# Kernel optimization log

Hardware: AMD Instinct MI355X
Metric: run time of the kernel (lower is better)

## Reference

```python
import jax, jax.numpy as jnp
import numpy as np

B, T = 16, 512          # batch, timesteps
IN = 16                 # input_path_dim
D = 128                 # cde_state_dim
H = 256                 # vf_hidden_dim
L = 136                 # logsig_size = 16 + 16*15/2 (depth-2 log-signature)
O = 32                  # output_path_dim


def _linear_params(key, out_f, in_f):
    kw, kb = jax.random.split(key)
    lim = 1.0 / np.sqrt(in_f)
    W = jax.random.uniform(kw, (out_f, in_f), minval=-lim, maxval=lim, dtype=jnp.float32)
    b = jax.random.uniform(kb, (out_f,), minval=-lim, maxval=lim, dtype=jnp.float32)
    return W, b


def setup_inputs() -> dict:
    key = jax.random.key(0)
    ks = jax.random.split(key, 10)
    x0 = jax.random.normal(ks[0], (B, IN), dtype=jnp.float32)
    # log-signature increments are small; scale down for numerical realism
    logsigs = jax.random.normal(ks[1], (B, T - 1, L), dtype=jnp.float32) * 0.01
    # initial MLP: IN -> H -> H -> D (softplus activations, linear final)
    iw1, ib1 = _linear_params(ks[2], H, IN)
    iw2, ib2 = _linear_params(ks[3], H, H)
    iw3, ib3 = _linear_params(ks[4], D, H)
    # vector-field MLP: D -> H -> H -> D*L (softplus, tanh final)
    fw1, fb1 = _linear_params(ks[5], H, D)
    fw2, fb2 = _linear_params(ks[6], H, H)
    fw3, fb3 = _linear_params(ks[7], D * L, H)
    # readout: D -> O
    rw, rb = _linear_params(ks[8], O, D)
    return dict(x0=x0, logsigs=logsigs,
                iw1=iw1, ib1=ib1, iw2=iw2, ib2=ib2, iw3=iw3, ib3=ib3,
                fw1=fw1, fb1=fb1, fw2=fw2, fb2=fb2, fw3=fw3, fb3=fb3,
                rw=rw, rb=rb)


def reference(x0, logsigs, iw1, ib1, iw2, ib2, iw3, ib3,
              fw1, fb1, fw2, fb2, fw3, fb3, rw, rb):
    sp = jax.nn.softplus
    # initial MLP -> h0: (B, D)
    h0 = sp(x0 @ iw1.T + ib1)
    h0 = sp(h0 @ iw2.T + ib2)
    h0 = h0 @ iw3.T + ib3

    def step(h, logsig_t):
        # vector-field MLP: (B, D) -> (B, D*L), tanh final activation
        z = sp(h @ fw1.T + fb1)
        z = sp(z @ fw2.T + fb2)
        z = jnp.tanh(z @ fw3.T + fb3)
        mat = z.reshape(h.shape[0], D, L)          # (B, D, L)
        h_next = h + jnp.einsum('bdl,bl->bd', mat, logsig_t)
        return h_next, h_next

    # scan over time: xs shape (T-1, B, L)
    _, h_hist = jax.lax.scan(step, h0, jnp.swapaxes(logsigs, 0, 1))
    h_all = jnp.concatenate([h0[None, :, :], h_hist], axis=0)  # (T, B, D)
    out = h_all @ rw.T + rb                                     # (T, B, O)
    return jnp.swapaxes(out, 0, 1)                              # (B, T, O)
```

## Files before the change

kernel.cpp:

```cpp
#include <hip/hip_runtime.h>

namespace {
constexpr int kB = 16, kT = 512, kIN = 16, kD = 128, kH = 256, kL = 136, kO = 32;
constexpr int kSteps = kT - 1;
constexpr int NBLK = 256;
constexpr int NTHR = 512;
constexpr int LH   = 68;
constexpr int NTILE = 5;
constexpr int FS   = 32;
constexpr int OFF_FW1 = 0;
constexpr int OFF_FW2 = 32768;
constexpr int OFF_AHI = 98304;
constexpr int OFF_ALO = 106752;
constexpr int OFF_DT  = 115200;
constexpr int OFF_OMS = 120576;
constexpr int OFF_Z1S = 124928;
constexpr int OFF_HB  = 125952;
constexpr int OFF_RED = 126464;
constexpr size_t LDS_BYTES = 126976;
}

typedef __attribute__((ext_vector_type(8))) short short8;
typedef __attribute__((ext_vector_type(4))) float f32x4;

__device__ __forceinline__ float softplusf(float x) {
  return fmaxf(x, 0.0f) + log1pf(expf(-fabsf(x)));
}
__device__ __forceinline__ unsigned short f2bf(float x) {
  unsigned u = __float_as_uint(x);
  return (unsigned short)((u + 0x7FFFu + ((u >> 16) & 1u)) >> 16);
}
__device__ __forceinline__ float bf2f(unsigned short h) {
  return __uint_as_float(((unsigned)h) << 16);
}
#define ALOADF(p)  __hip_atomic_load((p),  __ATOMIC_RELAXED, __HIP_MEMORY_SCOPE_AGENT)
#define ASTOREF(p,v) __hip_atomic_store((p), (v), __ATOMIC_RELAXED, __HIP_MEMORY_SCOPE_AGENT)

__global__ void __launch_bounds__(256)
rde_init(const float* __restrict__ x0,
         const float* __restrict__ iw1, const float* __restrict__ ib1,
         const float* __restrict__ iw2, const float* __restrict__ ib2,
         const float* __restrict__ iw3, const float* __restrict__ ib3,
         float* __restrict__ hist) {
  __shared__ float xs[kIN];
  __shared__ __align__(16) float t1[kH];
  __shared__ __align__(16) float t2[kH];
  const int b = blockIdx.x, tid = threadIdx.x;
  if (tid < kIN) xs[tid] = x0[b*kIN + tid];
  __syncthreads();
  {
    float a = ib1[tid];
#pragma unroll
    for (int i = 0; i < kIN; ++i) a = fmaf(xs[i], iw1[tid*kIN + i], a);
    t1[tid] = softplusf(a);
  }
  __syncthreads();
  {
    const float4* wr = (const float4*)(iw2 + (size_t)tid*kH);
    float a = ib2[tid];
#pragma unroll 8
    for (int q = 0; q < kH/4; ++q) {
      float4 w = wr[q];
      a = fmaf(t1[4*q+0], w.x, a); a = fmaf(t1[4*q+1], w.y, a);
      a = fmaf(t1[4*q+2], w.z, a); a = fmaf(t1[4*q+3], w.w, a);
    }
    t2[tid] = softplusf(a);
  }
  __syncthreads();
  if (tid < kD) {
    const float4* wr = (const float4*)(iw3 + (size_t)tid*kH);
    float a = ib3[tid];
#pragma unroll 8
    for (int q = 0; q < kH/4; ++q) {
      float4 w = wr[q];
      a = fmaf(t2[4*q+0], w.x, a); a = fmaf(t2[4*q+1], w.y, a);
      a = fmaf(t2[4*q+2], w.z, a); a = fmaf(t2[4*q+3], w.w, a);
    }
    hist[(size_t)b*kD + tid] = a;
  }
}

__global__ void __launch_bounds__(NTHR, 2)
rde_scan(const float* __restrict__ lsg,
         const float* __restrict__ fw1, const float* __restrict__ fb1,
         const float* __restrict__ fw2, const float* __restrict__ fb2,
         const float* __restrict__ fw3, const float* __restrict__ fb3,
         float* __restrict__ hist, float* z1g, float* z2g, float* partg,
         unsigned* z1fl, unsigned* z2fl, unsigned* pfl) {
  extern __shared__ char smem[];
  float* fw1s = (float*)(smem + OFF_FW1);
  float* fw2s = (float*)(smem + OFF_FW2);
  unsigned short* Ahi = (unsigned short*)(smem + OFF_AHI);
  unsigned short* Alo = (unsigned short*)(smem + OFF_ALO);
  float* Dt  = (float*)(smem + OFF_DT);
  float* oms = (float*)(smem + OFF_OMS);
  float* z1s = (float*)(smem + OFF_Z1S);
  float* hb  = (float*)(smem + OFF_HB);
  float* red = (float*)(smem + OFF_RED);

  const int tid  = threadIdx.x;
  const int k    = blockIdx.x;
  const int wave = tid >> 6, lane = tid & 63;
  const int d_own = k >> 1, l0 = (k & 1) * LH;
  const bool isMLP = (k < 64);
  const int bmlp = k >> 2, qm = k & 3, j0 = qm * 64;

  short8 bhi[8], blo[8];
  float biasv = 0.f;
  {
#pragma unroll
    for (int s = 0; s < 8; ++s) { bhi[s] = (short8)0; blo[s] = (short8)0; }
    if (wave < NTILE) {
      const int nl = wave*16 + (lane & 15);
      const int g  = lane >> 4;
      if (nl < LH) {
        const size_t row = (size_t)d_own*kL + l0 + nl;
        const float* wrow = fw3 + row*kH;
        biasv = fb3[row];
#pragma unroll
        for (int s = 0; s < 8; ++s) {
          const int k0 = s*32 + g*8;
          float4 v0 = *(const float4*)(wrow + k0);
          float4 v1 = *(const float4*)(wrow + k0 + 4);
          float vv[8] = {v0.x,v0.y,v0.z,v0.w,v1.x,v1.y,v1.z,v1.w};
#pragma unroll
          for (int e = 0; e < 8; ++e) {
            unsigned short hh = f2bf(vv[e]);
            bhi[s][e] = (short)hh;
            blo[s][e] = (short)f2bf(vv[e] - bf2f(hh));
          }
        }
      }
    }
  }
  float myfb1 = 0.f, myfb2 = 0.f;
  if (isMLP) {
    if (tid < 256) { int j = tid >> 2; myfb1 = fb1[j0 + j]; myfb2 = fb2[j0 + j]; }
    for (int i = tid; i < 64*32; i += NTHR) {
      int j = i >> 5, qq = i & 31;
      float4 v = *(const float4*)(fw1 + (size_t)(j0 + j)*kD + qq*4);
      fw1s[(qq*4+0)*64 + j] = v.x; fw1s[(qq*4+1)*64 + j] = v.y;
      fw1s[(qq*4+2)*64 + j] = v.z; fw1s[(qq*4+3)*64 + j] = v.w;
    }
    for (int i = tid; i < 64*64; i += NTHR) {
      int j = i >> 6, qq = i & 63;
      float4 v = *(const float4*)(fw2 + (size_t)(j0 + j)*kH + qq*4);
      fw2s[(qq*4+0)*64 + j] = v.x; fw2s[(qq*4+1)*64 + j] = v.y;
      fw2s[(qq*4+2)*64 + j] = v.z; fw2s[(qq*4+3)*64 + j] = v.w;
    }
    for (int i = tid; i < kD; i += NTHR) hb[i] = hist[(size_t)bmlp*kD + i];
  }
  __syncthreads();

  for (int t = 0; t < kSteps; ++t) {
    const unsigned epw = (unsigned)(t + 1);

    if (tid >= 256) {
      int c = tid - 256;
#pragma unroll 2
      for (int rep = 0; rep < 2; ++rep) {
        int cc = c + rep*256;
        if (cc < 272) {
          int bb = cc / 17, ii = cc % 17;
          float4 v = *(const float4*)(lsg + ((size_t)bb*kSteps + t)*kL + l0 + ii*4);
          *(float4*)(oms + bb*LH + ii*4) = v;
        }
      }
    }

    if (isMLP) {
      if (tid < 256) {
        int j = tid >> 2, ks = tid & 3;
        float a = 0.f;
#pragma unroll 8
        for (int kk = ks; kk < kD; kk += 4) a = fmaf(hb[kk], fw1s[kk*64 + j], a);
        a += __shfl_xor(a, 1); a += __shfl_xor(a, 2);
        if (ks == 0) ASTOREF(z1g + bmlp*kH + j0 + j, softplusf(a + myfb1));
      }
      __syncthreads();
      if (tid == 0) __hip_atomic_store(z1fl + (bmlp*4 + qm)*FS, epw,
                                       __ATOMIC_RELAXED, __HIP_MEMORY_SCOPE_AGENT);
      if (tid < 4) {
        while (__hip_atomic_load(z1fl + (bmlp*4 + tid)*FS, __ATOMIC_RELAXED,
                                 __HIP_MEMORY_SCOPE_AGENT) < epw)
          __builtin_amdgcn_s_sleep(1);
      }
      __syncthreads();
      asm volatile("" ::: "memory");
      if (tid < 128) {
        unsigned long long v = __hip_atomic_load((const unsigned long long*)(z1g + bmlp*kH) + tid,
                                                 __ATOMIC_RELAXED, __HIP_MEMORY_SCOPE_AGENT);
        union { unsigned long long u; float2 f; } cv; cv.u = v;
        z1s[2*tid] = cv.f.x; z1s[2*tid + 1] = cv.f.y;
      }
      __syncthreads();
      if (tid < 256) {
        int j = tid >> 2, ks = tid & 3;
        float a = 0.f;
#pragma unroll 8
        for (int kk = ks; kk < kH; kk += 4) a = fmaf(z1s[kk], fw2s[kk*64 + j], a);
        a += __shfl_xor(a, 1); a += __shfl_xor(a, 2);
        if (ks == 0) ASTOREF(z2g + bmlp*kH + j0 + j, softplusf(a + myfb2));
      }
      __syncthreads();
      if (tid == 0) __hip_atomic_store(z2fl + (bmlp*4 + qm)*FS, epw,
                                       __ATOMIC_RELAXED, __HIP_MEMORY_SCOPE_AGENT);
    }

    if (tid < 64) {
      while (__hip_atomic_load(z2fl + tid*FS, __ATOMIC_RELAXED,
                               __HIP_MEMORY_SCOPE_AGENT) < epw)
        __builtin_amdgcn_s_sleep(2);
    }
    __syncthreads();
    asm volatile("" ::: "memory");
#pragma unroll
    for (int i = 0; i < 4; ++i) {
      int p = tid*4 + i;
      unsigned long long v = __hip_atomic_load((const unsigned long long*)z2g + p,
                                               __ATOMIC_RELAXED, __HIP_MEMORY_SCOPE_AGENT);
      union { unsigned long long u; float2 f; } cv; cv.u = v;
      int m = p >> 7, kk = (p & 127) * 2;
      unsigned short h0 = f2bf(cv.f.x), h1 = f2bf(cv.f.y);
      unsigned short e0 = f2bf(cv.f.x - bf2f(h0)), e1 = f2bf(cv.f.y - bf2f(h1));
      *(unsigned*)(Ahi + m*264 + kk) = (unsigned)h0 | ((unsigned)h1 << 16);
      *(unsigned*)(Alo + m*264 + kk) = (unsigned)e0 | ((unsigned)e1 << 16);
    }
    __syncthreads();

    if (wave < NTILE) {
      f32x4 acc = {biasv, biasv, biasv, biasv};
      const unsigned short* arh = Ahi + (lane & 15)*264;
      const unsigned short* arl = Alo + (lane & 15)*264;
      const int g = lane >> 4;
#pragma unroll
      for (int s = 0; s < 8; ++s) {
        short8 ah = *(const short8*)(arh + s*32 + g*8);
        short8 al = *(const short8*)(arl + s*32 + g*8);
        acc = __builtin_amdgcn_mfma_f32_16x16x32_bf16(ah, bhi[s], acc, 0, 0, 0);
        acc = __builtin_amdgcn_mfma_f32_16x16x32_bf16(ah, blo[s], acc, 0, 0, 0);
        acc = __builtin_amdgcn_mfma_f32_16x16x32_bf16(al, bhi[s], acc, 0, 0, 0);
      }
#pragma unroll
      for (int r = 0; r < 4; ++r)
        Dt[(g*4 + r)*84 + wave*16 + (lane & 15)] = acc[r];
    }
    __syncthreads();

    {
      const int b3 = tid & 15, lb = tid >> 4;
      float p = tanhf(Dt[b3*84 + lb     ]) * oms[b3*LH + lb     ]
              + tanhf(Dt[b3*84 + lb + 32]) * oms[b3*LH + lb + 32];
      if (lb < 4)
        p += tanhf(Dt[b3*84 + lb + 64]) * oms[b3*LH + lb + 64];
      p += __shfl_xor(p, 16); p += __shfl_xor(p, 32);
      if (lane < 16) red[lane*8 + wave] = p;
    }
    __syncthreads();
    if (tid < 16) {
      float s = 0.f;
#pragma unroll
      for (int j = 0; j < 8; ++j) s += red[tid*8 + j];
      ASTOREF(partg + tid*256 + k, s);
    }
    __syncthreads();
    if (tid == 0) __hip_atomic_store(pfl + k*FS, epw,
                                     __ATOMIC_RELAXED, __HIP_MEMORY_SCOPE_AGENT);

    if (isMLP) {
      if (tid < 256) {
        while (__hip_atomic_load(pfl + tid*FS, __ATOMIC_RELAXED,
                                 __HIP_MEMORY_SCOPE_AGENT) < epw)
          __builtin_amdgcn_s_sleep(2);
      }
      __syncthreads();
      asm volatile("" ::: "memory");
      if (tid < 128) {
        unsigned long long v = __hip_atomic_load((const unsigned long long*)(partg + bmlp*256) + tid,
                                                 __ATOMIC_RELAXED, __HIP_MEMORY_SCOPE_AGENT);
        union { unsigned long long u; float2 f; } cv; cv.u = v;
        hb[tid] += cv.f.x + cv.f.y;
      }
      __syncthreads();
      if (qm == 0 && tid < 128)
        hist[((size_t)(t+1)*kB + bmlp)*kD + tid] = hb[tid];
    }
  }
}

__global__ void __launch_bounds__(512)
rde_readout(const float* __restrict__ hist, const float* __restrict__ rw,
            const float* __restrict__ rb, float* __restrict__ out) {
  const int t = blockIdx.x, tid = threadIdx.x;
  const int b = tid >> 5, o = tid & 31;
  const float4* hr = (const float4*)(hist + ((size_t)t*kB + b)*kD);
  const float4* wr = (const float4*)(rw + (size_t)o*kD);
  float a = rb[o];
#pragma unroll 8
  for (int q = 0; q < kD/4; ++q) {
    float4 h4 = hr[q], w4 = wr[q];
    a = fmaf(h4.x,w4.x,a); a = fmaf(h4.y,w4.y,a);
    a = fmaf(h4.z,w4.z,a); a = fmaf(h4.w,w4.w,a);
  }
  out[((size_t)b*kT + t)*kO + o] = a;
}

extern "C" void kernel_launch(void* const* d_in, const int* in_sizes, int n_in,
                              void* d_out, int out_size, void* d_ws, size_t ws_size,
                              hipStream_t stream) {
  const float* x0  = (const float*)d_in[0];
  const float* lsg = (const float*)d_in[1];
  const float* iw1 = (const float*)d_in[2];
  const float* ib1 = (const float*)d_in[3];
  const float* iw2 = (const float*)d_in[4];
  const float* ib2 = (const float*)d_in[5];
  const float* iw3 = (const float*)d_in[6];
  const float* ib3 = (const float*)d_in[7];
  const float* fw1 = (const float*)d_in[8];
  const float* fb1 = (const float*)d_in[9];
  const float* fw2 = (const float*)d_in[10];
  const float* fb2 = (const float*)d_in[11];
  const float* fw3 = (const float*)d_in[12];
  const float* fb3 = (const float*)d_in[13];
  const float* rw  = (const float*)d_in[14];
  const float* rb  = (const float*)d_in[15];
  float* out = (float*)d_out;

  float*    hist  = (float*)d_ws;
  float*    z1g   = hist + (size_t)kT*kB*kD;
  float*    z2g   = z1g + kB*kH;
  float*    partg = z2g + kB*kH;
  unsigned* z1fl  = (unsigned*)(partg + kB*NBLK);
  unsigned* z2fl  = z1fl + 64*FS;
  unsigned* pfl   = z2fl + 64*FS;

  hipMemsetAsync(z1fl, 0, (size_t)(64 + 64 + 256)*FS*sizeof(unsigned), stream);
  hipFuncSetAttribute((const void*)rde_scan,
                      hipFuncAttributeMaxDynamicSharedMemorySize, (int)LDS_BYTES);

  rde_init<<<kB, 256, 0, stream>>>(x0, iw1, ib1, iw2, ib2, iw3, ib3, hist);

  void* args[] = { (void*)&lsg, (void*)&fw1, (void*)&fb1, (void*)&fw2, (void*)&fb2,
                   (void*)&fw3, (void*)&fb3, (void*)&hist, (void*)&z1g, (void*)&z2g,
                   (void*)&partg, (void*)&z1fl, (void*)&z2fl, (void*)&pfl };
  hipLaunchCooperativeKernel((const void*)rde_scan, dim3(NBLK), dim3(NTHR),
                             args, (unsigned)LDS_BYTES, stream);

  rde_readout<<<kT, 512, 0, stream>>>(hist, rw, rb, out);
}
```

Before: 4.503 ms.

## Pack epoch tags with data to replace flag handshakes in cooperative scan

Intermediate z1 values and partial sums are now written as 64-bit words that pair the value with its epoch. Consumers poll the data directly instead of waiting on separate flag arrays, which removes a flag-store barrier and a dependent round trip per exchange. The MLP blocks now spread their matvecs over all 512 threads using a padded float2 weight layout. The MLP blocks also pre-split z2 into bf16 hi/lo pairs, so consumer blocks only repack it. This raises LDS use to about 137 KB per block, which may limit the two-blocks-per-CU launch bound, and it doubles the polled traffic for the tagged arrays.

```diff
diff --git a/kernel.cpp b/kernel.cpp
--- a/kernel.cpp
+++ b/kernel.cpp
@@ -7,21 +7,23 @@
 constexpr int NTHR = 512;
 constexpr int LH   = 68;
 constexpr int NTILE = 5;
-constexpr int FS   = 32;
 constexpr int OFF_FW1 = 0;
-constexpr int OFF_FW2 = 32768;
-constexpr int OFF_AHI = 98304;
-constexpr int OFF_ALO = 106752;
-constexpr int OFF_DT  = 115200;
-constexpr int OFF_OMS = 120576;
-constexpr int OFF_Z1S = 124928;
-constexpr int OFF_HB  = 125952;
-constexpr int OFF_RED = 126464;
-constexpr size_t LDS_BYTES = 126976;
+constexpr int OFF_FW2 = 36864;
+constexpr int OFF_AHI = 110592;
+constexpr int OFF_ALO = 119040;
+constexpr int OFF_DT  = 127488;
+constexpr int OFF_OMS = 132864;
+constexpr int OFF_Z1S = 137216;
+constexpr int OFF_HB  = 138240;
+constexpr int OFF_HINC= 138752;
+constexpr int OFF_RED = 139264;
+constexpr size_t LDS_BYTES = 139776;
 }
 
 typedef __attribute__((ext_vector_type(8))) short short8;
 typedef __attribute__((ext_vector_type(4))) float f32x4;
+
+union PK { unsigned long long u; struct { float v; unsigned ep; } s; };
 
 __device__ __forceinline__ float softplusf(float x) {
   return fmaxf(x, 0.0f) + log1pf(expf(-fabsf(x)));
@@ -33,8 +35,6 @@
 __device__ __forceinline__ float bf2f(unsigned short h) {
   return __uint_as_float(((unsigned)h) << 16);
 }
-#define ALOADF(p)  __hip_atomic_load((p),  __ATOMIC_RELAXED, __HIP_MEMORY_SCOPE_AGENT)
-#define ASTOREF(p,v) __hip_atomic_store((p), (v), __ATOMIC_RELAXED, __HIP_MEMORY_SCOPE_AGENT)
 
 __global__ void __launch_bounds__(256)
 rde_init(const float* __restrict__ x0,
@@ -85,18 +85,20 @@
          const float* __restrict__ fw1, const float* __restrict__ fb1,
          const float* __restrict__ fw2, const float* __restrict__ fb2,
          const float* __restrict__ fw3, const float* __restrict__ fb3,
-         float* __restrict__ hist, float* z1g, float* z2g, float* partg,
-         unsigned* z1fl, unsigned* z2fl, unsigned* pfl) {
+         float* __restrict__ hist,
+         unsigned long long* z1x, unsigned* z2x, unsigned* z2snt,
+         unsigned long long* partx) {
   extern __shared__ char smem[];
   float* fw1s = (float*)(smem + OFF_FW1);
   float* fw2s = (float*)(smem + OFF_FW2);
   unsigned short* Ahi = (unsigned short*)(smem + OFF_AHI);
   unsigned short* Alo = (unsigned short*)(smem + OFF_ALO);
-  float* Dt  = (float*)(smem + OFF_DT);
-  float* oms = (float*)(smem + OFF_OMS);
-  float* z1s = (float*)(smem + OFF_Z1S);
-  float* hb  = (float*)(smem + OFF_HB);
-  float* red = (float*)(smem + OFF_RED);
+  float* Dt   = (float*)(smem + OFF_DT);
+  float* oms  = (float*)(smem + OFF_OMS);
+  float* z1s  = (float*)(smem + OFF_Z1S);
+  float* hb   = (float*)(smem + OFF_HB);
+  float* hinc = (float*)(smem + OFF_HINC);
+  float* red  = (float*)(smem + OFF_RED);
 
   const int tid  = threadIdx.x;
   const int k    = blockIdx.x;
@@ -104,6 +106,7 @@
   const int d_own = k >> 1, l0 = (k & 1) * LH;
   const bool isMLP = (k < 64);
   const int bmlp = k >> 2, qm = k & 3, j0 = qm * 64;
+  const int jj = tid >> 3, ks = tid & 7;
 
   short8 bhi[8], blo[8];
   float biasv = 0.f;
@@ -135,18 +138,18 @@
   }
   float myfb1 = 0.f, myfb2 = 0.f;
   if (isMLP) {
-    if (tid < 256) { int j = tid >> 2; myfb1 = fb1[j0 + j]; myfb2 = fb2[j0 + j]; }
+    myfb1 = fb1[j0 + jj]; myfb2 = fb2[j0 + jj];
     for (int i = tid; i < 64*32; i += NTHR) {
-      int j = i >> 5, qq = i & 31;
-      float4 v = *(const float4*)(fw1 + (size_t)(j0 + j)*kD + qq*4);
-      fw1s[(qq*4+0)*64 + j] = v.x; fw1s[(qq*4+1)*64 + j] = v.y;
-      fw1s[(qq*4+2)*64 + j] = v.z; fw1s[(qq*4+3)*64 + j] = v.w;
+      int j = i >> 5, q = i & 31;
+      float4 v = *(const float4*)(fw1 + (size_t)(j0 + j)*kD + q*4);
+      *(float2*)(fw1s + (2*q  )*144 + 2*j) = make_float2(v.x, v.y);
+      *(float2*)(fw1s + (2*q+1)*144 + 2*j) = make_float2(v.z, v.w);
     }
     for (int i = tid; i < 64*64; i += NTHR) {
-      int j = i >> 6, qq = i & 63;
-      float4 v = *(const float4*)(fw2 + (size_t)(j0 + j)*kH + qq*4);
-      fw2s[(qq*4+0)*64 + j] = v.x; fw2s[(qq*4+1)*64 + j] = v.y;
-      fw2s[(qq*4+2)*64 + j] = v.z; fw2s[(qq*4+3)*64 + j] = v.w;
+      int j = i >> 6, q = i & 63;
+      float4 v = *(const float4*)(fw2 + (size_t)(j0 + j)*kH + q*4);
+      *(float2*)(fw2s + (2*q  )*144 + 2*j) = make_float2(v.x, v.y);
+      *(float2*)(fw2s + (2*q+1)*144 + 2*j) = make_float2(v.z, v.w);
     }
     for (int i = tid; i < kD; i += NTHR) hb[i] = hist[(size_t)bmlp*kD + i];
   }
@@ -155,76 +158,112 @@
   for (int t = 0; t < kSteps; ++t) {
     const unsigned epw = (unsigned)(t + 1);
 
-    if (tid >= 256) {
-      int c = tid - 256;
+    if (!isMLP) {
+      if (tid >= 256) {
+        int c = tid - 256;
 #pragma unroll 2
-      for (int rep = 0; rep < 2; ++rep) {
-        int cc = c + rep*256;
-        if (cc < 272) {
-          int bb = cc / 17, ii = cc % 17;
-          float4 v = *(const float4*)(lsg + ((size_t)bb*kSteps + t)*kL + l0 + ii*4);
-          *(float4*)(oms + bb*LH + ii*4) = v;
-        }
-      }
-    }
-
-    if (isMLP) {
-      if (tid < 256) {
-        int j = tid >> 2, ks = tid & 3;
+        for (int rep = 0; rep < 2; ++rep) {
+          int cc = c + rep*256;
+          if (cc < 272) {
+            int bb = cc / 17, ii = cc % 17;
+            float4 v = *(const float4*)(lsg + ((size_t)bb*kSteps + t)*kL + l0 + ii*4);
+            *(float4*)(oms + bb*LH + ii*4) = v;
+          }
+        }
+      }
+    } else {
+      {
         float a = 0.f;
-#pragma unroll 8
-        for (int kk = ks; kk < kD; kk += 4) a = fmaf(hb[kk], fw1s[kk*64 + j], a);
-        a += __shfl_xor(a, 1); a += __shfl_xor(a, 2);
-        if (ks == 0) ASTOREF(z1g + bmlp*kH + j0 + j, softplusf(a + myfb1));
-      }
-      __syncthreads();
-      if (tid == 0) __hip_atomic_store(z1fl + (bmlp*4 + qm)*FS, epw,
-                                       __ATOMIC_RELAXED, __HIP_MEMORY_SCOPE_AGENT);
-      if (tid < 4) {
-        while (__hip_atomic_load(z1fl + (bmlp*4 + tid)*FS, __ATOMIC_RELAXED,
-                                 __HIP_MEMORY_SCOPE_AGENT) < epw)
-          __builtin_amdgcn_s_sleep(1);
+#pragma unroll
+        for (int kh = ks; kh < 64; kh += 8) {
+          float2 w  = *(const float2*)(fw1s + kh*144 + 2*jj);
+          float2 h2 = *(const float2*)(hb + 2*kh);
+          a = fmaf(h2.x, w.x, a); a = fmaf(h2.y, w.y, a);
+        }
+        a += __shfl_xor(a, 1); a += __shfl_xor(a, 2); a += __shfl_xor(a, 4);
+        if (ks == 0) {
+          PK p; p.s.v = softplusf(a + myfb1); p.s.ep = epw;
+          __hip_atomic_store(z1x + bmlp*kH + j0 + jj, p.u,
+                             __ATOMIC_RELAXED, __HIP_MEMORY_SCOPE_AGENT);
+        }
+      }
+      if (tid >= 256) {
+        int c = tid - 256;
+#pragma unroll 2
+        for (int rep = 0; rep < 2; ++rep) {
+          int cc = c + rep*256;
+          if (cc < 272) {
+            int bb = cc / 17, ii = cc % 17;
+            float4 v = *(const float4*)(lsg + ((size_t)bb*kSteps + t)*kL + l0 + ii*4);
+            *(float4*)(oms + bb*LH + ii*4) = v;
+          }
+        }
+      }
+      if (tid < 128) {
+#pragma unroll
+        for (int s = 0; s < 2; ++s) {
+          int idx = tid*2 + s;
+          PK q;
+          for (;;) {
+            q.u = __hip_atomic_load(z1x + bmlp*kH + idx,
+                                    __ATOMIC_RELAXED, __HIP_MEMORY_SCOPE_AGENT);
+            if (q.s.ep == epw) break;
+            __builtin_amdgcn_s_sleep(1);
+          }
+          z1s[idx] = q.s.v;
+        }
       }
       __syncthreads();
       asm volatile("" ::: "memory");
-      if (tid < 128) {
-        unsigned long long v = __hip_atomic_load((const unsigned long long*)(z1g + bmlp*kH) + tid,
-                                                 __ATOMIC_RELAXED, __HIP_MEMORY_SCOPE_AGENT);
-        union { unsigned long long u; float2 f; } cv; cv.u = v;
-        z1s[2*tid] = cv.f.x; z1s[2*tid + 1] = cv.f.y;
+      {
+        float a = 0.f;
+#pragma unroll
+        for (int kh = ks; kh < 128; kh += 8) {
+          float2 w  = *(const float2*)(fw2s + kh*144 + 2*jj);
+          float2 z2v = *(const float2*)(z1s + 2*kh);
+          a = fmaf(z2v.x, w.x, a); a = fmaf(z2v.y, w.y, a);
+        }
+        a += __shfl_xor(a, 1); a += __shfl_xor(a, 2); a += __shfl_xor(a, 4);
+        if (ks == 0) {
+          float v = softplusf(a + myfb2);
+          unsigned short hh = f2bf(v);
+          unsigned short ll = f2bf(v - bf2f(hh));
+          __hip_atomic_store(z2x + bmlp*kH + j0 + jj,
+                             (unsigned)hh | ((unsigned)ll << 16),
+                             __ATOMIC_RELAXED, __HIP_MEMORY_SCOPE_AGENT);
+        }
       }
       __syncthreads();
-      if (tid < 256) {
-        int j = tid >> 2, ks = tid & 3;
-        float a = 0.f;
-#pragma unroll 8
-        for (int kk = ks; kk < kH; kk += 4) a = fmaf(z1s[kk], fw2s[kk*64 + j], a);
-        a += __shfl_xor(a, 1); a += __shfl_xor(a, 2);
-        if (ks == 0) ASTOREF(z2g + bmlp*kH + j0 + j, softplusf(a + myfb2));
-      }
-      __syncthreads();
-      if (tid == 0) __hip_atomic_store(z2fl + (bmlp*4 + qm)*FS, epw,
+      if (tid == 0)
+        __hip_atomic_store(z2snt + (bmlp*4 + qm)*32, epw,
+                           __ATOMIC_RELAXED, __HIP_MEMORY_SCOPE_AGENT);
+    }
+
+    if (tid < 64) {
+      for (;;) {
+        unsigned e = __hip_atomic_load(z2snt + tid*32,
                                        __ATOMIC_RELAXED, __HIP_MEMORY_SCOPE_AGENT);
-    }
-
-    if (tid < 64) {
-      while (__hip_atomic_load(z2fl + tid*FS, __ATOMIC_RELAXED,
-                               __HIP_MEMORY_SCOPE_AGENT) < epw)
+        if (e == epw) break;
         __builtin_amdgcn_s_sleep(2);
+      }
     }
     __syncthreads();
     asm volatile("" ::: "memory");
-#pragma unroll
-    for (int i = 0; i < 4; ++i) {
-      int p = tid*4 + i;
-      unsigned long long v = __hip_atomic_load((const unsigned long long*)z2g + p,
-                                               __ATOMIC_RELAXED, __HIP_MEMORY_SCOPE_AGENT);
-      union { unsigned long long u; float2 f; } cv; cv.u = v;
-      int m = p >> 7, kk = (p & 127) * 2;
-      unsigned short h0 = f2bf(cv.f.x), h1 = f2bf(cv.f.y);
-      unsigned short e0 = f2bf(cv.f.x - bf2f(h0)), e1 = f2bf(cv.f.y - bf2f(h1));
-      *(unsigned*)(Ahi + m*264 + kk) = (unsigned)h0 | ((unsigned)h1 << 16);
-      *(unsigned*)(Alo + m*264 + kk) = (unsigned)e0 | ((unsigned)e1 << 16);
+    {
+      unsigned pk[8];
+      const unsigned* src = z2x + tid*8;
+#pragma unroll
+      for (int i = 0; i < 8; ++i)
+        pk[i] = __hip_atomic_load(src + i, __ATOMIC_RELAXED, __HIP_MEMORY_SCOPE_AGENT);
+      const int e0 = tid*8, m = e0 >> 8, kk = e0 & 255;
+      unsigned short* ph = Ahi + m*264 + kk;
+      unsigned short* pl = Alo + m*264 + kk;
+#pragma unroll
+      for (int i = 0; i < 4; ++i) {
+        unsigned a = pk[2*i], b = pk[2*i+1];
+        *(unsigned*)(ph + 2*i) = (a & 0xffffu) | (b << 16);
+        *(unsigned*)(pl + 2*i) = (a >> 16) | (b & 0xffff0000u);
+      }
     }
     __syncthreads();
 
@@ -261,29 +300,32 @@
       float s = 0.f;
 #pragma unroll
       for (int j = 0; j < 8; ++j) s += red[tid*8 + j];
-      ASTOREF(partg + tid*256 + k, s);
-    }
-    __syncthreads();
-    if (tid == 0) __hip_atomic_store(pfl + k*FS, epw,
-                                     __ATOMIC_RELAXED, __HIP_MEMORY_SCOPE_AGENT);
+      PK p; p.s.v = s; p.s.ep = epw;
+      __hip_atomic_store(partx + tid*NBLK + k, p.u,
+                         __ATOMIC_RELAXED, __HIP_MEMORY_SCOPE_AGENT);
+    }
 
     if (isMLP) {
+      float pval = 0.f;
       if (tid < 256) {
-        while (__hip_atomic_load(pfl + tid*FS, __ATOMIC_RELAXED,
-                                 __HIP_MEMORY_SCOPE_AGENT) < epw)
+        PK q;
+        for (;;) {
+          q.u = __hip_atomic_load(partx + bmlp*NBLK + tid,
+                                  __ATOMIC_RELAXED, __HIP_MEMORY_SCOPE_AGENT);
+          if (q.s.ep == epw) break;
           __builtin_amdgcn_s_sleep(2);
+        }
+        pval = q.s.v;
+        float p2 = pval + __shfl_xor(pval, 1);
+        if ((tid & 1) == 0) hinc[tid >> 1] = p2;
       }
       __syncthreads();
-      asm volatile("" ::: "memory");
       if (tid < 128) {
-        unsigned long long v = __hip_atomic_load((const unsigned long long*)(partg + bmlp*256) + tid,
-                                                 __ATOMIC_RELAXED, __HIP_MEMORY_SCOPE_AGENT);
-        union { unsigned long long u; float2 f; } cv; cv.u = v;
-        hb[tid] += cv.f.x + cv.f.y;
+        float hn = hb[tid] + hinc[tid];
+        hb[tid] = hn;
+        if (qm == 0) hist[((size_t)(t+1)*kB + bmlp)*kD + tid] = hn;
       }
       __syncthreads();
-      if (qm == 0 && tid < 128)
-        hist[((size_t)(t+1)*kB + bmlp)*kD + tid] = hb[tid];
     }
   }
 }
@@ -326,23 +368,22 @@
   const float* rb  = (const float*)d_in[15];
   float* out = (float*)d_out;
 
-  float*    hist  = (float*)d_ws;
-  float*    z1g   = hist + (size_t)kT*kB*kD;
-  float*    z2g   = z1g + kB*kH;
-  float*    partg = z2g + kB*kH;
-  unsigned* z1fl  = (unsigned*)(partg + kB*NBLK);
-  unsigned* z2fl  = z1fl + 64*FS;
-  unsigned* pfl   = z2fl + 64*FS;
-
-  hipMemsetAsync(z1fl, 0, (size_t)(64 + 64 + 256)*FS*sizeof(unsigned), stream);
+  float* hist = (float*)d_ws;
+  unsigned long long* z1x = (unsigned long long*)(hist + (size_t)kT*kB*kD);
+  unsigned* z2x   = (unsigned*)(z1x + kB*kH);
+  unsigned* z2snt = z2x + kB*kH;
+  unsigned long long* partx = (unsigned long long*)(z2snt + 64*32);
+
+  size_t xbytes = (size_t)kB*kH*8 + (size_t)kB*kH*4 + 64*32*4 + (size_t)kB*NBLK*8;
+  hipMemsetAsync(z1x, 0, xbytes, stream);
   hipFuncSetAttribute((const void*)rde_scan,
                       hipFuncAttributeMaxDynamicSharedMemorySize, (int)LDS_BYTES);
 
   rde_init<<<kB, 256, 0, stream>>>(x0, iw1, ib1, iw2, ib2, iw3, ib3, hist);
 
   void* args[] = { (void*)&lsg, (void*)&fw1, (void*)&fb1, (void*)&fw2, (void*)&fb2,
-                   (void*)&fw3, (void*)&fb3, (void*)&hist, (void*)&z1g, (void*)&z2g,
-                   (void*)&partg, (void*)&z1fl, (void*)&z2fl, (void*)&pfl };
+                   (void*)&fw3, (void*)&fb3, (void*)&hist, (void*)&z1x, (void*)&z2x,
+                   (void*)&z2snt, (void*)&partx };
   hipLaunchCooperativeKernel((const void*)rde_scan, dim3(NBLK), dim3(NTHR),
                              args, (unsigned)LDS_BYTES, stream);
 
```

Measured after the change: 4.777 ms. 1.06x slower.
